# Kernel optimization log

Measured on AMD Instinct MI355X. Metric: run time of the kernel, lower is better.

The kernel has to match this reference:

```python
import jax, jax.numpy as jnp
import numpy as np

NEG_SLOPE = 0.2


def setup_inputs() -> dict:
    key = jax.random.key(0)
    kx, ka, kW, kav = jax.random.split(key, 4)
    B, V, H, D = 8, 2048, 256, 128
    x = jax.random.normal(kx, (B, V, H), dtype=jnp.float32)
    adjacency_matrix = jax.random.randint(ka, (V, V), 0, 2, dtype=jnp.int32)
    W = jax.random.normal(kW, (D, H), dtype=jnp.float32) * 0.05  # Linear(H->D), weight [out,in]
    a = jax.random.normal(kav, (1, 2 * D), dtype=jnp.float32) * 0.05  # Linear(2D->1)
    return {"x": x, "adjacency_matrix": adjacency_matrix, "W": W, "a": a}


def reference(x, adjacency_matrix, W, a):
    B, V, H = x.shape
    D = W.shape[0]
    # p = W(x): [B,V,D]
    p = jnp.einsum('bvh,dh->bvd', x, W)
    # a(cat(p_i, p_j)) == a_left.p_i + a_right.p_j ; leaky_relu applied to the sum (same math,
    # avoids materializing the O(B*V^2*2D) repeat/concat tensor)
    a_left, a_right = a[0, :D], a[0, D:]
    e_i = p @ a_left    # [B,V]
    e_j = p @ a_right   # [B,V]
    scores = jax.nn.leaky_relu(e_i[:, :, None] + e_j[:, None, :], negative_slope=NEG_SLOPE)  # [B,V,V]
    weights = jax.nn.softmax(scores, axis=-1)
    adj = adjacency_matrix.astype(weights.dtype)[None]  # [1,V,V]
    weights_masked = weights * adj
    # renormalize masked weights to the (unmasked) row mass
    weights_masked = weights_masked * (
        jnp.sum(weights, axis=-1, keepdims=True) / jnp.sum(weights_masked, axis=-1, keepdims=True)
    )
    # weighted sum over neighbors j: sum_j w[b,i,j] * p[b,j,:]
    attentioned = jnp.einsum('bij,bjd->bid', weights_masked, p)
    return jax.nn.relu(attentioned)
```

## Files before the change

### kernel.cpp

```cpp
#include <hip/hip_runtime.h>
#include <hip/hip_bf16.h>

#define BATCH 8
#define V 2048
#define H 256
#define D 128

typedef __attribute__((ext_vector_type(8))) _Float16 f16x8;
typedef __attribute__((ext_vector_type(4))) float f32x4;
typedef unsigned int uint32;

static __device__ __forceinline__ uint32 pk2(float lo, float hi) {
  __fp16 __attribute__((ext_vector_type(2))) h = __builtin_amdgcn_cvt_pkrtz(lo, hi);
  uint32 u;
  __builtin_memcpy(&u, &h, 4);
  return u;
}

__global__ __launch_bounds__(256) void k_pack(const int* __restrict__ adj,
                                              const float* __restrict__ W,
                                              const float* __restrict__ a,
                                              unsigned int* __restrict__ pkT,
                                              float* __restrict__ vL,
                                              float* __restrict__ vR) {
  const int blk = blockIdx.x;
  if (blk < V) {
    const int w = threadIdx.x >> 6, lane = threadIdx.x & 63;
    const int* row = adj + (size_t)blk * V;
#pragma unroll
    for (int it = 0; it < 8; ++it) {
      const int j = it * 256 + w * 64 + lane;
      unsigned long long m = __ballot(row[j] != 0);
      if (lane < 2) {
        const int jw = it * 8 + w * 2 + lane;
        pkT[(size_t)jw * V + blk] = (unsigned int)(m >> (lane * 32));
      }
    }
  } else {
    const int h = threadIdx.x;
    float sL = 0.f, sR = 0.f;
    for (int d = 0; d < D; ++d) {
      const float wv = W[(size_t)d * H + h];
      sL += wv * a[d];
      sR += wv * a[D + d];
    }
    vL[h] = sL;
    vR[h] = sR;
  }
}

#define DOT4(s, xv, vv) \
  s += (xv).x * (vv).x + (xv).y * (vv).y + (xv).z * (vv).z + (xv).w * (vv).w;

__global__ __launch_bounds__(256, 2) void k_proj(const float* __restrict__ x,
                                                 const float* __restrict__ W,
                                                 const float* __restrict__ vL,
                                                 const float* __restrict__ vR,
                                                 _Float16* __restrict__ pTf,
                                                 float* __restrict__ ei,
                                                 _Float16* __restrict__ Fh,
                                                 _Float16* __restrict__ Ph) {
  __shared__ _Float16 st[128][52];
  const int t = threadIdx.x, lane = t & 63, wave = t >> 6;
  const int b = blockIdx.x >> 6;
  const int j0 = (blockIdx.x & 63) * 32;
  const int kq = lane >> 4, l15 = lane & 15;

  const float* wrow0 = W + (size_t)(wave * 32 + l15) * H + kq * 8;
  const float* wrow1 = wrow0 + 16 * H;
  const float* xrow0 = x + ((size_t)(b * V + j0 + l15)) * H + kq * 8;
  const float* xrow1 = xrow0 + 16 * H;
  const float* vLp = vL + kq * 8;
  const float* vRp = vR + kq * 8;

  f32x4 acc[2][2];
#pragma unroll
  for (int i_ = 0; i_ < 2; ++i_)
#pragma unroll
    for (int j_ = 0; j_ < 2; ++j_) acc[i_][j_] = (f32x4){0.f, 0.f, 0.f, 0.f};
  float eL0 = 0.f, eL1 = 0.f, eR0 = 0.f, eR1 = 0.f;

  typedef union { uint32 u[4]; f16x8 v; } AFu_;
#pragma unroll
  for (int ks = 0; ks < 8; ++ks) {
    const int ho = ks * 32;
    const float4 w0a = *(const float4*)(wrow0 + ho), w0b = *(const float4*)(wrow0 + ho + 4);
    const float4 w1a = *(const float4*)(wrow1 + ho), w1b = *(const float4*)(wrow1 + ho + 4);
    const float4 x0a = *(const float4*)(xrow0 + ho), x0b = *(const float4*)(xrow0 + ho + 4);
    const float4 x1a = *(const float4*)(xrow1 + ho), x1b = *(const float4*)(xrow1 + ho + 4);
    AFu_ aw0, aw1, bx0, bx1;
    aw0.u[0] = pk2(w0a.x, w0a.y); aw0.u[1] = pk2(w0a.z, w0a.w);
    aw0.u[2] = pk2(w0b.x, w0b.y); aw0.u[3] = pk2(w0b.z, w0b.w);
    aw1.u[0] = pk2(w1a.x, w1a.y); aw1.u[1] = pk2(w1a.z, w1a.w);
    aw1.u[2] = pk2(w1b.x, w1b.y); aw1.u[3] = pk2(w1b.z, w1b.w);
    bx0.u[0] = pk2(x0a.x, x0a.y); bx0.u[1] = pk2(x0a.z, x0a.w);
    bx0.u[2] = pk2(x0b.x, x0b.y); bx0.u[3] = pk2(x0b.z, x0b.w);
    bx1.u[0] = pk2(x1a.x, x1a.y); bx1.u[1] = pk2(x1a.z, x1a.w);
    bx1.u[2] = pk2(x1b.x, x1b.y); bx1.u[3] = pk2(x1b.z, x1b.w);
    acc[0][0] = __builtin_amdgcn_mfma_f32_16x16x32_f16(aw0.v, bx0.v, acc[0][0], 0, 0, 0);
    acc[0][1] = __builtin_amdgcn_mfma_f32_16x16x32_f16(aw0.v, bx1.v, acc[0][1], 0, 0, 0);
    acc[1][0] = __builtin_amdgcn_mfma_f32_16x16x32_f16(aw1.v, bx0.v, acc[1][0], 0, 0, 0);
    acc[1][1] = __builtin_amdgcn_mfma_f32_16x16x32_f16(aw1.v, bx1.v, acc[1][1], 0, 0, 0);
    if (wave == 0) {
      const float4 vla = *(const float4*)(vLp + ho), vlb = *(const float4*)(vLp + ho + 4);
      const float4 vra = *(const float4*)(vRp + ho), vrb = *(const float4*)(vRp + ho + 4);
      DOT4(eL0, x0a, vla) DOT4(eL0, x0b, vlb)
      DOT4(eL1, x1a, vla) DOT4(eL1, x1b, vlb)
      DOT4(eR0, x0a, vra) DOT4(eR0, x0b, vrb)
      DOT4(eR1, x1a, vra) DOT4(eR1, x1b, vrb)
    }
  }

  if (wave == 0) {
    eL0 += __shfl_xor(eL0, 16, 64); eL0 += __shfl_xor(eL0, 32, 64);
    eL1 += __shfl_xor(eL1, 16, 64); eL1 += __shfl_xor(eL1, 32, 64);
    eR0 += __shfl_xor(eR0, 16, 64); eR0 += __shfl_xor(eR0, 32, 64);
    eR1 += __shfl_xor(eR1, 16, 64); eR1 += __shfl_xor(eR1, 32, 64);
    if (lane < 16) {
      const size_t r0 = (size_t)b * V + j0 + lane;
      ei[r0] = eL0;
      Fh[r0] = (_Float16)__expf(eR0);
      Ph[r0] = (_Float16)__expf(0.2f * eR0);
      const size_t r1 = r0 + 16;
      ei[r1] = eL1;
      Fh[r1] = (_Float16)__expf(eR1);
      Ph[r1] = (_Float16)__expf(0.2f * eR1);
    }
  }

#pragma unroll
  for (int t_ = 0; t_ < 2; ++t_)
#pragma unroll
    for (int jt = 0; jt < 2; ++jt)
#pragma unroll
      for (int r = 0; r < 4; ++r)
        st[(wave * 2 + t_) * 16 + kq * 4 + r][jt * 16 + l15] = (_Float16)acc[t_][jt][r];
  __syncthreads();

  const int c = (blockIdx.x & 63) >> 1;
  const int ks = blockIdx.x & 1;
  const int g = t >> 6;
#pragma unroll
  for (int ff = 0; ff < 2; ++ff) {
    const int dt = ff * 4 + g;
    const int dR = dt * 16 + l15;
    const int jc = kq * 8;
    union { unsigned long long ll[2]; f16x8 v; } vv_;
    vv_.ll[0] = *(const unsigned long long*)&st[dR][jc];
    vv_.ll[1] = *(const unsigned long long*)&st[dR][jc + 4];
    *(f16x8*)((char*)pTf +
              (((((size_t)b * 32 + c) * 8 + dt) * 2 + ks) * 64 + lane) * 16) = vv_.v;
  }
}


typedef union { uint4 v; uint32 u[4]; } U4;
typedef union { uint32 u[4]; f16x8 v; } AFu;
struct PFS {
  U4 FH0, FH1, PH0, PH1;
  uint32 w[2][2];
  AFu AF[2][2];
};

#define PKMUL(d, a, b) asm("v_pk_mul_f16 %0, %1, %2" : "=v"(d) : "v"(a), "v"(b));
#define PKMAX(d, a, b) asm("v_pk_max_f16 %0, %1, %2" : "=v"(d) : "v"(a), "v"(b));

#define WGEN(S)                                                        \
  _Pragma("unroll") for (int ig_ = 0; ig_ < 2; ++ig_) {                \
    const uint32 E2_ = Ei2g[ig_], EP2_ = Eip2g[ig_];                   \
    _Pragma("unroll") for (int ks_ = 0; ks_ < 2; ++ks_) {              \
      U4 M_;                                                           \
      M_.v = lut[((S).w[ig_][ks_] >> kq8) & 0xFF];                     \
      const U4& FH_ = ks_ ? (S).FH1 : (S).FH0;                         \
      const U4& PH_ = ks_ ? (S).PH1 : (S).PH0;                         \
      _Pragma("unroll") for (int p_ = 0; p_ < 4; ++p_) {               \
        uint32 t0_, t1_;                                               \
        PKMUL(t0_, E2_, FH_.u[p_])                                     \
        PKMUL(t1_, EP2_, PH_.u[p_])                                    \
        PKMAX(t0_, t0_, t1_)                                           \
        (S).AF[ig_][ks_].u[p_] = t0_ & M_.u[p_];                       \
      }                                                                \
    }                                                                  \
  }

#define PFETCH(S, C)                                       \
  {                                                        \
    const char* f_ = fbase + (C) * 128 + kq16;             \
    const char* p_ = pbase + (C) * 128 + kq16;             \
    (S).FH0.v = *(const uint4*)(f_);                       \
    (S).FH1.v = *(const uint4*)(f_ + 64);                  \
    (S).PH0.v = *(const uint4*)(p_);                       \
    (S).PH1.v = *(const uint4*)(p_ + 64);                  \
    (S).w[0][0] = adjpT[(size_t)((C) * 2) * V + iR0];      \
    (S).w[0][1] = adjpT[(size_t)((C) * 2 + 1) * V + iR0];  \
    (S).w[1][0] = adjpT[(size_t)((C) * 2) * V + iR1];      \
    (S).w[1][1] = adjpT[(size_t)((C) * 2 + 1) * V + iR1];  \
  }

#define LOADB(BR, C)                                      \
  {                                                       \
    const char* g_ = gbase + (size_t)(C) * 16384;         \
    _Pragma("unroll") for (int q_ = 0; q_ < 4; ++q_)      \
      BR[q_] = *(const f16x8*)(g_ + q_ * 1024);           \
  }

#define DOMFMA(S, BX)                                                          \
  _Pragma("unroll") for (int ig_ = 0; ig_ < 2; ++ig_)                          \
    _Pragma("unroll") for (int nt_ = 0; nt_ < 2; ++nt_)                        \
      _Pragma("unroll") for (int ks_ = 0; ks_ < 2; ++ks_)                      \
        acc[ig_][nt_][ks_] = __builtin_amdgcn_mfma_f32_16x16x32_f16(           \
            (S).AF[ig_][ks_].v, BX[nt_ * 2 + ks_], acc[ig_][nt_][ks_], 0, 0, 0); \
  _Pragma("unroll") for (int ig_ = 0; ig_ < 2; ++ig_)                          \
    _Pragma("unroll") for (int ks_ = 0; ks_ < 2; ++ks_)                        \
      accS[ig_][ks_] = __builtin_amdgcn_mfma_f32_16x16x32_f16(                 \
          (S).AF[ig_][ks_].v, onesv, accS[ig_][ks_], 0, 0, 0);

#define BODYF(C, SX, BX, SY)   \
  {                            \
    DOMFMA(SX, BX)             \
    WGEN(SY)                   \
    LOADB(BX, (C) + 2)         \
    PFETCH(SX, (C) + 2)        \
  }

__global__ __launch_bounds__(256, 2) void k_attn(
    const _Float16* __restrict__ pTf,
    const float* __restrict__ ei,
    const _Float16* __restrict__ Fht,
    const _Float16* __restrict__ Pht,
    const unsigned int* __restrict__ adjpT,
    float* __restrict__ out) {
  __shared__ uint4 lut[256];
  {
    const int tb = threadIdx.x;
    const uint32 m0 = ((tb & 1) ? 0xFFFFu : 0u) | ((tb & 2) ? 0xFFFF0000u : 0u);
    const uint32 m1 = ((tb & 4) ? 0xFFFFu : 0u) | ((tb & 8) ? 0xFFFF0000u : 0u);
    const uint32 m2 = ((tb & 16) ? 0xFFFFu : 0u) | ((tb & 32) ? 0xFFFF0000u : 0u);
    const uint32 m3 = ((tb & 64) ? 0xFFFFu : 0u) | ((tb & 128) ? 0xFFFF0000u : 0u);
    lut[tb] = make_uint4(m0, m1, m2, m3);
  }
  __syncthreads();

  const int t = threadIdx.x, lane = t & 63, wave = t >> 6;
  const int ih = wave >> 1;
  const int dq = wave & 1;
  const int pay = (blockIdx.x & 7) * 64 + (blockIdx.x >> 3);
  const int bdh = pay >> 4;
  const int itl = pay & 15;
  const int b = bdh >> 2, dh = (bdh >> 1) & 1;
  const int it = ((bdh & 1) << 4) | itl;
  const int i0b = it * 64;
  const int kq = lane >> 4;
  const int kq8 = kq * 8;
  const int kq16 = kq * 16;
  const int l15 = lane & 15;
  const int ibase = i0b + ih * 32;
  const int iR0 = ibase + l15;
  const int iR1 = iR0 + 16;

  const float eiv0 = ei[(size_t)b * V + iR0];
  const float eiv1 = ei[(size_t)b * V + iR1];
  uint32 Ei2g[2], Eip2g[2];
  {
    const float e0 = __expf(eiv0), e1 = __expf(eiv1);
    const float p0 = __expf(0.2f * eiv0), p1 = __expf(0.2f * eiv1);
    Ei2g[0] = pk2(e0, e0); Ei2g[1] = pk2(e1, e1);
    Eip2g[0] = pk2(p0, p0); Eip2g[1] = pk2(p1, p1);
  }
  const char* fbase = (const char*)(Fht + (size_t)b * V);
  const char* pbase = (const char*)(Pht + (size_t)b * V);
  const size_t fb0 = ((size_t)b * 32) * 16384 + (size_t)dh * 8192;
  const char* gbase = (const char*)pTf + fb0 + dq * 4096 + lane * 16;

  union { uint32 u[4]; f16x8 v; } ones_;
  ones_.u[0] = ones_.u[1] = ones_.u[2] = ones_.u[3] = 0x3C003C00u;
  const f16x8 onesv = ones_.v;

  f32x4 acc[2][2][2];
#pragma unroll
  for (int a_ = 0; a_ < 2; ++a_)
#pragma unroll
    for (int b_ = 0; b_ < 2; ++b_)
#pragma unroll
      for (int c_ = 0; c_ < 2; ++c_) acc[a_][b_][c_] = (f32x4){0.f, 0.f, 0.f, 0.f};
  f32x4 accS[2][2];
#pragma unroll
  for (int a_ = 0; a_ < 2; ++a_)
#pragma unroll
    for (int c_ = 0; c_ < 2; ++c_) accS[a_][c_] = (f32x4){0.f, 0.f, 0.f, 0.f};

  f16x8 bA[4], bB[4];
  PFS sA, sB;

  LOADB(bA, 0)
  LOADB(bB, 1)
  PFETCH(sA, 0)
  PFETCH(sB, 1)
  WGEN(sA)

  for (int c2 = 0; c2 < 15; ++c2) {
    const int c = c2 * 2;
    BODYF(c, sA, bA, sB)
    BODYF(c + 1, sB, bB, sA)
  }
  {
    DOMFMA(sA, bA)
    WGEN(sB)
  }
  { DOMFMA(sB, bB) }

  float* ob = out + ((size_t)b * V + ibase) * D + dh * 64 + dq * 32 + l15;
#pragma unroll
  for (int ig = 0; ig < 2; ++ig) {
#pragma unroll
    for (int r = 0; r < 4; ++r) {
      const float inv_ = 1.0f / (accS[ig][0][r] + accS[ig][1][r]);
#pragma unroll
      for (int nt = 0; nt < 2; ++nt) {
        const float v = (acc[ig][nt][0][r] + acc[ig][nt][1][r]) * inv_;
        ob[(size_t)(ig * 16 + kq * 4 + r) * D + nt * 16] = fmaxf(v, 0.f);
      }
    }
  }
}

extern "C" void kernel_launch(void* const* d_in, const int* in_sizes, int n_in,
                              void* d_out, int out_size, void* d_ws, size_t ws_size,
                              hipStream_t stream) {
  const float* x = (const float*)d_in[0];
  const int* adj = (const int*)d_in[1];
  const float* W = (const float*)d_in[2];
  const float* a = (const float*)d_in[3];
  float* out = (float*)d_out;

  char* ws = (char*)d_ws;
  _Float16* pTf = (_Float16*)ws;
  float* ei = (float*)(ws + (4u << 20));
  _Float16* Fh = (_Float16*)(ws + (4u << 20) + 65536);
  _Float16* Ph = (_Float16*)(ws + (4u << 20) + 98304);
  unsigned int* adjpT = (unsigned int*)(ws + (4u << 20) + 131072);
  float* vL = (float*)(ws + (4u << 20) + 131072 + 524288);
  float* vR = (float*)(ws + (4u << 20) + 131072 + 524288 + 1024);

  k_pack<<<dim3(V + 1), dim3(256), 0, stream>>>(adj, W, a, adjpT, vL, vR);
  k_proj<<<dim3(BATCH * (V / 32)), dim3(256), 0, stream>>>(x, W, vL, vR, pTf, ei, Fh, Ph);
  k_attn<<<dim3(BATCH * 2 * (V / 64)), dim3(256), 0, stream>>>(pTf, ei, Fh, Ph, adjpT, out);
}
```

Before: 54.69 us.

## Stage x in swizzled LDS, pre-convert W to fp16, shrink attention tiles

k_pack gains an extra block that converts W to fp16 once, so k_proj loads fp16 W fragments and no longer converts W per block. k_proj loads x coalesced into an XOR-swizzled LDS tile, computing the e_i/e_j dot products with full-wave reductions during staging. k_attn now gives each wave its own 16-column slice of a 32-row tile, with twice as many blocks, and computes the weight fragments just before use instead of software-pipelining them. Occupancy is raised to 4 blocks per CU, which trades recomputing the masked-weight fragments in every wave for lower register pressure and more parallelism.

```diff
diff --git a/kernel.cpp b/kernel.cpp
--- a/kernel.cpp
+++ b/kernel.cpp
@@ -22,7 +22,8 @@
                                               const float* __restrict__ a,
                                               unsigned int* __restrict__ pkT,
                                               float* __restrict__ vL,
-                                              float* __restrict__ vR) {
+                                              float* __restrict__ vR,
+                                              _Float16* __restrict__ Wh) {
   const int blk = blockIdx.x;
   if (blk < V) {
     const int w = threadIdx.x >> 6, lane = threadIdx.x & 63;
@@ -36,7 +37,7 @@
         pkT[(size_t)jw * V + blk] = (unsigned int)(m >> (lane * 32));
       }
     }
-  } else {
+  } else if (blk == V) {
     const int h = threadIdx.x;
     float sL = 0.f, sR = 0.f;
     for (int d = 0; d < D; ++d) {
@@ -46,86 +47,80 @@
     }
     vL[h] = sL;
     vR[h] = sR;
-  }
-}
-
-#define DOT4(s, xv, vv) \
-  s += (xv).x * (vv).x + (xv).y * (vv).y + (xv).z * (vv).z + (xv).w * (vv).w;
+  } else {
+    const int t = threadIdx.x;
+    for (int i = 0; i < D; ++i)
+      Wh[(size_t)i * H + t] = (_Float16)W[(size_t)i * H + t];
+  }
+}
 
 __global__ __launch_bounds__(256, 2) void k_proj(const float* __restrict__ x,
-                                                 const float* __restrict__ W,
+                                                 const _Float16* __restrict__ Wh,
                                                  const float* __restrict__ vL,
                                                  const float* __restrict__ vR,
                                                  _Float16* __restrict__ pTf,
                                                  float* __restrict__ ei,
                                                  _Float16* __restrict__ Fh,
                                                  _Float16* __restrict__ Ph) {
+  __shared__ char xls[32 * 512];
   __shared__ _Float16 st[128][52];
   const int t = threadIdx.x, lane = t & 63, wave = t >> 6;
   const int b = blockIdx.x >> 6;
-  const int j0 = (blockIdx.x & 63) * 32;
+  const int jt0 = blockIdx.x & 63;
+  const int j0 = jt0 * 32;
   const int kq = lane >> 4, l15 = lane & 15;
 
-  const float* wrow0 = W + (size_t)(wave * 32 + l15) * H + kq * 8;
-  const float* wrow1 = wrow0 + 16 * H;
-  const float* xrow0 = x + ((size_t)(b * V + j0 + l15)) * H + kq * 8;
-  const float* xrow1 = xrow0 + 16 * H;
-  const float* vLp = vL + kq * 8;
-  const float* vRp = vR + kq * 8;
+  {
+    const float4 vl4 = *(const float4*)(vL + lane * 4);
+    const float4 vr4 = *(const float4*)(vR + lane * 4);
+#pragma unroll
+    for (int rr = 0; rr < 8; ++rr) {
+      const int row = wave * 8 + rr;
+      const float4 xv = *(const float4*)(x + ((size_t)(b * V + j0 + row)) * H + lane * 4);
+      uint32 u0 = pk2(xv.x, xv.y), u1 = pk2(xv.z, xv.w);
+      const int off = row * 512 + ((lane * 8) ^ ((row & 7) << 4));
+      *(uint32*)(xls + off) = u0;
+      *(uint32*)(xls + off + 4) = u1;
+      float eL = xv.x * vl4.x + xv.y * vl4.y + xv.z * vl4.z + xv.w * vl4.w;
+      float eR = xv.x * vr4.x + xv.y * vr4.y + xv.z * vr4.z + xv.w * vr4.w;
+#pragma unroll
+      for (int off_ = 1; off_ < 64; off_ <<= 1) {
+        eL += __shfl_xor(eL, off_, 64);
+        eR += __shfl_xor(eR, off_, 64);
+      }
+      if (lane == 0) {
+        const size_t r_ = (size_t)b * V + j0 + row;
+        ei[r_] = eL;
+        Fh[r_] = (_Float16)__expf(eR);
+        Ph[r_] = (_Float16)__expf(0.2f * eR);
+      }
+    }
+  }
+  __syncthreads();
 
   f32x4 acc[2][2];
 #pragma unroll
   for (int i_ = 0; i_ < 2; ++i_)
 #pragma unroll
     for (int j_ = 0; j_ < 2; ++j_) acc[i_][j_] = (f32x4){0.f, 0.f, 0.f, 0.f};
-  float eL0 = 0.f, eL1 = 0.f, eR0 = 0.f, eR1 = 0.f;
-
-  typedef union { uint32 u[4]; f16x8 v; } AFu_;
+
+  const char* wbase = (const char*)Wh + ((size_t)(wave * 32 + l15) * H + kq * 8) * 2;
 #pragma unroll
   for (int ks = 0; ks < 8; ++ks) {
-    const int ho = ks * 32;
-    const float4 w0a = *(const float4*)(wrow0 + ho), w0b = *(const float4*)(wrow0 + ho + 4);
-    const float4 w1a = *(const float4*)(wrow1 + ho), w1b = *(const float4*)(wrow1 + ho + 4);
-    const float4 x0a = *(const float4*)(xrow0 + ho), x0b = *(const float4*)(xrow0 + ho + 4);
-    const float4 x1a = *(const float4*)(xrow1 + ho), x1b = *(const float4*)(xrow1 + ho + 4);
-    AFu_ aw0, aw1, bx0, bx1;
-    aw0.u[0] = pk2(w0a.x, w0a.y); aw0.u[1] = pk2(w0a.z, w0a.w);
-    aw0.u[2] = pk2(w0b.x, w0b.y); aw0.u[3] = pk2(w0b.z, w0b.w);
-    aw1.u[0] = pk2(w1a.x, w1a.y); aw1.u[1] = pk2(w1a.z, w1a.w);
-    aw1.u[2] = pk2(w1b.x, w1b.y); aw1.u[3] = pk2(w1b.z, w1b.w);
-    bx0.u[0] = pk2(x0a.x, x0a.y); bx0.u[1] = pk2(x0a.z, x0a.w);
-    bx0.u[2] = pk2(x0b.x, x0b.y); bx0.u[3] = pk2(x0b.z, x0b.w);
-    bx1.u[0] = pk2(x1a.x, x1a.y); bx1.u[1] = pk2(x1a.z, x1a.w);
-    bx1.u[2] = pk2(x1b.x, x1b.y); bx1.u[3] = pk2(x1b.z, x1b.w);
-    acc[0][0] = __builtin_amdgcn_mfma_f32_16x16x32_f16(aw0.v, bx0.v, acc[0][0], 0, 0, 0);
-    acc[0][1] = __builtin_amdgcn_mfma_f32_16x16x32_f16(aw0.v, bx1.v, acc[0][1], 0, 0, 0);
-    acc[1][0] = __builtin_amdgcn_mfma_f32_16x16x32_f16(aw1.v, bx0.v, acc[1][0], 0, 0, 0);
-    acc[1][1] = __builtin_amdgcn_mfma_f32_16x16x32_f16(aw1.v, bx1.v, acc[1][1], 0, 0, 0);
-    if (wave == 0) {
-      const float4 vla = *(const float4*)(vLp + ho), vlb = *(const float4*)(vLp + ho + 4);
-      const float4 vra = *(const float4*)(vRp + ho), vrb = *(const float4*)(vRp + ho + 4);
-      DOT4(eL0, x0a, vla) DOT4(eL0, x0b, vlb)
-      DOT4(eL1, x1a, vla) DOT4(eL1, x1b, vlb)
-      DOT4(eR0, x0a, vra) DOT4(eR0, x0b, vrb)
-      DOT4(eR1, x1a, vra) DOT4(eR1, x1b, vrb)
-    }
-  }
-
-  if (wave == 0) {
-    eL0 += __shfl_xor(eL0, 16, 64); eL0 += __shfl_xor(eL0, 32, 64);
-    eL1 += __shfl_xor(eL1, 16, 64); eL1 += __shfl_xor(eL1, 32, 64);
-    eR0 += __shfl_xor(eR0, 16, 64); eR0 += __shfl_xor(eR0, 32, 64);
-    eR1 += __shfl_xor(eR1, 16, 64); eR1 += __shfl_xor(eR1, 32, 64);
-    if (lane < 16) {
-      const size_t r0 = (size_t)b * V + j0 + lane;
-      ei[r0] = eL0;
-      Fh[r0] = (_Float16)__expf(eR0);
-      Ph[r0] = (_Float16)__expf(0.2f * eR0);
-      const size_t r1 = r0 + 16;
-      ei[r1] = eL1;
-      Fh[r1] = (_Float16)__expf(eR1);
-      Ph[r1] = (_Float16)__expf(0.2f * eR1);
-    }
+    f16x8 aw[2], bx[2];
+#pragma unroll
+    for (int t_ = 0; t_ < 2; ++t_)
+      aw[t_] = *(const f16x8*)(wbase + (t_ * 16 * H + ks * 32) * 2);
+#pragma unroll
+    for (int jt = 0; jt < 2; ++jt) {
+      const int row = jt * 16 + l15;
+      bx[jt] = *(const f16x8*)(xls + row * 512 + ((ks * 64 + kq * 16) ^ ((l15 & 7) << 4)));
+    }
+#pragma unroll
+    for (int t_ = 0; t_ < 2; ++t_)
+#pragma unroll
+      for (int jt = 0; jt < 2; ++jt)
+        acc[t_][jt] = __builtin_amdgcn_mfma_f32_16x16x32_f16(aw[t_], bx[jt], acc[t_][jt], 0, 0, 0);
   }
 
 #pragma unroll
@@ -137,8 +132,8 @@
         st[(wave * 2 + t_) * 16 + kq * 4 + r][jt * 16 + l15] = (_Float16)acc[t_][jt][r];
   __syncthreads();
 
-  const int c = (blockIdx.x & 63) >> 1;
-  const int ks = blockIdx.x & 1;
+  const int c = jt0 >> 1;
+  const int ksh = jt0 & 1;
   const int g = t >> 6;
 #pragma unroll
   for (int ff = 0; ff < 2; ++ff) {
@@ -149,28 +144,26 @@
     vv_.ll[0] = *(const unsigned long long*)&st[dR][jc];
     vv_.ll[1] = *(const unsigned long long*)&st[dR][jc + 4];
     *(f16x8*)((char*)pTf +
-              (((((size_t)b * 32 + c) * 8 + dt) * 2 + ks) * 64 + lane) * 16) = vv_.v;
-  }
-}
-
+              (((((size_t)b * 32 + c) * 8 + dt) * 2 + ksh) * 64 + lane) * 16) = vv_.v;
+  }
+}
 
 typedef union { uint4 v; uint32 u[4]; } U4;
 typedef union { uint32 u[4]; f16x8 v; } AFu;
 struct PFS {
   U4 FH0, FH1, PH0, PH1;
   uint32 w[2][2];
-  AFu AF[2][2];
 };
 
 #define PKMUL(d, a, b) asm("v_pk_mul_f16 %0, %1, %2" : "=v"(d) : "v"(a), "v"(b));
 #define PKMAX(d, a, b) asm("v_pk_max_f16 %0, %1, %2" : "=v"(d) : "v"(a), "v"(b));
 
-#define WGEN(S)                                                        \
+#define WGENX(S, AF_)                                                  \
   _Pragma("unroll") for (int ig_ = 0; ig_ < 2; ++ig_) {                \
     const uint32 E2_ = Ei2g[ig_], EP2_ = Eip2g[ig_];                   \
     _Pragma("unroll") for (int ks_ = 0; ks_ < 2; ++ks_) {              \
       U4 M_;                                                           \
-      M_.v = lut[((S).w[ig_][ks_] >> kq8) & 0xFF];                     \
+      M_.v = lut[(((S).w[ig_][ks_]) >> kq8) & 0xFF];                   \
       const U4& FH_ = ks_ ? (S).FH1 : (S).FH0;                         \
       const U4& PH_ = ks_ ? (S).PH1 : (S).PH0;                         \
       _Pragma("unroll") for (int p_ = 0; p_ < 4; ++p_) {               \
@@ -178,52 +171,58 @@
         PKMUL(t0_, E2_, FH_.u[p_])                                     \
         PKMUL(t1_, EP2_, PH_.u[p_])                                    \
         PKMAX(t0_, t0_, t1_)                                           \
-        (S).AF[ig_][ks_].u[p_] = t0_ & M_.u[p_];                       \
+        AF_[ig_][ks_].u[p_] = t0_ & M_.u[p_];                          \
       }                                                                \
     }                                                                  \
   }
 
-#define PFETCH(S, C)                                       \
-  {                                                        \
-    const char* f_ = fbase + (C) * 128 + kq16;             \
-    const char* p_ = pbase + (C) * 128 + kq16;             \
-    (S).FH0.v = *(const uint4*)(f_);                       \
-    (S).FH1.v = *(const uint4*)(f_ + 64);                  \
-    (S).PH0.v = *(const uint4*)(p_);                       \
-    (S).PH1.v = *(const uint4*)(p_ + 64);                  \
-    (S).w[0][0] = adjpT[(size_t)((C) * 2) * V + iR0];      \
-    (S).w[0][1] = adjpT[(size_t)((C) * 2 + 1) * V + iR0];  \
-    (S).w[1][0] = adjpT[(size_t)((C) * 2) * V + iR1];      \
-    (S).w[1][1] = adjpT[(size_t)((C) * 2 + 1) * V + iR1];  \
-  }
-
-#define LOADB(BR, C)                                      \
-  {                                                       \
-    const char* g_ = gbase + (size_t)(C) * 16384;         \
-    _Pragma("unroll") for (int q_ = 0; q_ < 4; ++q_)      \
-      BR[q_] = *(const f16x8*)(g_ + q_ * 1024);           \
-  }
-
-#define DOMFMA(S, BX)                                                          \
+#define PFETCH(S, C)                                           \
+  {                                                            \
+    const char* f_ = fbase + (C) * 128 + kq16;                 \
+    const char* p_ = pbase + (C) * 128 + kq16;                 \
+    (S).FH0.v = *(const uint4*)(f_);                           \
+    (S).FH1.v = *(const uint4*)(f_ + 64);                      \
+    (S).PH0.v = *(const uint4*)(p_);                           \
+    (S).PH1.v = *(const uint4*)(p_ + 64);                      \
+    (S).w[0][0] = adjpT[(size_t)((C) * 2) * V + iR0];          \
+    (S).w[0][1] = adjpT[(size_t)((C) * 2 + 1) * V + iR0];      \
+    (S).w[1][0] = adjpT[(size_t)((C) * 2) * V + iR1];          \
+    (S).w[1][1] = adjpT[(size_t)((C) * 2 + 1) * V + iR1];      \
+  }
+
+#define LOADB(BR, C)                                  \
+  {                                                   \
+    const char* g_ = gbase + (size_t)(C) * 16384;     \
+    BR[0] = *(const f16x8*)(g_);                      \
+    BR[1] = *(const f16x8*)(g_ + 1024);               \
+  }
+
+#define DOMFMA(AF_, BX)                                                        \
   _Pragma("unroll") for (int ig_ = 0; ig_ < 2; ++ig_)                          \
-    _Pragma("unroll") for (int nt_ = 0; nt_ < 2; ++nt_)                        \
-      _Pragma("unroll") for (int ks_ = 0; ks_ < 2; ++ks_)                      \
-        acc[ig_][nt_][ks_] = __builtin_amdgcn_mfma_f32_16x16x32_f16(           \
-            (S).AF[ig_][ks_].v, BX[nt_ * 2 + ks_], acc[ig_][nt_][ks_], 0, 0, 0); \
-  _Pragma("unroll") for (int ig_ = 0; ig_ < 2; ++ig_)                          \
-    _Pragma("unroll") for (int ks_ = 0; ks_ < 2; ++ks_)                        \
+    _Pragma("unroll") for (int ks_ = 0; ks_ < 2; ++ks_) {                      \
+      acc[ig_][ks_] = __builtin_amdgcn_mfma_f32_16x16x32_f16(                  \
+          AF_[ig_][ks_].v, BX[ks_], acc[ig_][ks_], 0, 0, 0);                   \
       accS[ig_][ks_] = __builtin_amdgcn_mfma_f32_16x16x32_f16(                 \
-          (S).AF[ig_][ks_].v, onesv, accS[ig_][ks_], 0, 0, 0);
-
-#define BODYF(C, SX, BX, SY)   \
-  {                            \
-    DOMFMA(SX, BX)             \
-    WGEN(SY)                   \
-    LOADB(BX, (C) + 2)         \
-    PFETCH(SX, (C) + 2)        \
-  }
-
-__global__ __launch_bounds__(256, 2) void k_attn(
+          AF_[ig_][ks_].v, onesv, accS[ig_][ks_], 0, 0, 0);                    \
+    }
+
+#define BODYF(C, S, BX)       \
+  {                           \
+    AFu af_[2][2];            \
+    WGENX(S, af_)             \
+    DOMFMA(af_, BX)           \
+    LOADB(BX, (C) + 2)        \
+    PFETCH(S, (C) + 2)        \
+  }
+
+#define BODYT(S, BX)          \
+  {                           \
+    AFu af_[2][2];            \
+    WGENX(S, af_)             \
+    DOMFMA(af_, BX)           \
+  }
+
+__global__ __launch_bounds__(256, 4) void k_attn(
     const _Float16* __restrict__ pTf,
     const float* __restrict__ ei,
     const _Float16* __restrict__ Fht,
@@ -241,21 +240,18 @@
   }
   __syncthreads();
 
-  const int t = threadIdx.x, lane = t & 63, wave = t >> 6;
-  const int ih = wave >> 1;
-  const int dq = wave & 1;
-  const int pay = (blockIdx.x & 7) * 64 + (blockIdx.x >> 3);
-  const int bdh = pay >> 4;
-  const int itl = pay & 15;
-  const int b = bdh >> 2, dh = (bdh >> 1) & 1;
-  const int it = ((bdh & 1) << 4) | itl;
-  const int i0b = it * 64;
+  const int t = threadIdx.x, lane = t & 63;
+  const int dq = t >> 6;
+  const int pay = (blockIdx.x & 7) * 128 + (blockIdx.x >> 3);
+  const int b = pay >> 7;
+  const int dh = (pay >> 6) & 1;
+  const int it = pay & 63;
+  const int i0 = it * 32;
   const int kq = lane >> 4;
   const int kq8 = kq * 8;
   const int kq16 = kq * 16;
   const int l15 = lane & 15;
-  const int ibase = i0b + ih * 32;
-  const int iR0 = ibase + l15;
+  const int iR0 = i0 + l15;
   const int iR1 = iR0 + 16;
 
   const float eiv0 = ei[(size_t)b * V + iR0];
@@ -269,57 +265,47 @@
   }
   const char* fbase = (const char*)(Fht + (size_t)b * V);
   const char* pbase = (const char*)(Pht + (size_t)b * V);
-  const size_t fb0 = ((size_t)b * 32) * 16384 + (size_t)dh * 8192;
-  const char* gbase = (const char*)pTf + fb0 + dq * 4096 + lane * 16;
+  const char* gbase = (const char*)pTf + ((size_t)b * 32) * 16384 +
+                      (size_t)(dh * 4 + dq) * 2048 + lane * 16;
 
   union { uint32 u[4]; f16x8 v; } ones_;
   ones_.u[0] = ones_.u[1] = ones_.u[2] = ones_.u[3] = 0x3C003C00u;
   const f16x8 onesv = ones_.v;
 
-  f32x4 acc[2][2][2];
+  f32x4 acc[2][2];
+  f32x4 accS[2][2];
 #pragma unroll
   for (int a_ = 0; a_ < 2; ++a_)
 #pragma unroll
-    for (int b_ = 0; b_ < 2; ++b_)
-#pragma unroll
-      for (int c_ = 0; c_ < 2; ++c_) acc[a_][b_][c_] = (f32x4){0.f, 0.f, 0.f, 0.f};
-  f32x4 accS[2][2];
-#pragma unroll
-  for (int a_ = 0; a_ < 2; ++a_)
-#pragma unroll
-    for (int c_ = 0; c_ < 2; ++c_) accS[a_][c_] = (f32x4){0.f, 0.f, 0.f, 0.f};
-
-  f16x8 bA[4], bB[4];
+    for (int c_ = 0; c_ < 2; ++c_) {
+      acc[a_][c_] = (f32x4){0.f, 0.f, 0.f, 0.f};
+      accS[a_][c_] = (f32x4){0.f, 0.f, 0.f, 0.f};
+    }
+
+  f16x8 bA[2], bB[2];
   PFS sA, sB;
 
   LOADB(bA, 0)
   LOADB(bB, 1)
   PFETCH(sA, 0)
   PFETCH(sB, 1)
-  WGEN(sA)
 
   for (int c2 = 0; c2 < 15; ++c2) {
     const int c = c2 * 2;
-    BODYF(c, sA, bA, sB)
-    BODYF(c + 1, sB, bB, sA)
-  }
-  {
-    DOMFMA(sA, bA)
-    WGEN(sB)
-  }
-  { DOMFMA(sB, bB) }
-
-  float* ob = out + ((size_t)b * V + ibase) * D + dh * 64 + dq * 32 + l15;
+    BODYF(c, sA, bA)
+    BODYF(c + 1, sB, bB)
+  }
+  BODYT(sA, bA)
+  BODYT(sB, bB)
+
+  float* ob = out + ((size_t)b * V + i0) * D + dh * 64 + dq * 16 + l15;
 #pragma unroll
   for (int ig = 0; ig < 2; ++ig) {
 #pragma unroll
     for (int r = 0; r < 4; ++r) {
       const float inv_ = 1.0f / (accS[ig][0][r] + accS[ig][1][r]);
-#pragma unroll
-      for (int nt = 0; nt < 2; ++nt) {
-        const float v = (acc[ig][nt][0][r] + acc[ig][nt][1][r]) * inv_;
-        ob[(size_t)(ig * 16 + kq * 4 + r) * D + nt * 16] = fmaxf(v, 0.f);
-      }
+      const float v = (acc[ig][0][r] + acc[ig][1][r]) * inv_;
+      ob[(size_t)(ig * 16 + kq * 4 + r) * D] = fmaxf(v, 0.f);
     }
   }
 }
@@ -339,10 +325,11 @@
   _Float16* Fh = (_Float16*)(ws + (4u << 20) + 65536);
   _Float16* Ph = (_Float16*)(ws + (4u << 20) + 98304);
   unsigned int* adjpT = (unsigned int*)(ws + (4u << 20) + 131072);
-  float* vL = (float*)(ws + (4u << 20) + 131072 + 524288);
-  float* vR = (float*)(ws + (4u << 20) + 131072 + 524288 + 1024);
-
-  k_pack<<<dim3(V + 1), dim3(256), 0, stream>>>(adj, W, a, adjpT, vL, vR);
-  k_proj<<<dim3(BATCH * (V / 32)), dim3(256), 0, stream>>>(x, W, vL, vR, pTf, ei, Fh, Ph);
-  k_attn<<<dim3(BATCH * 2 * (V / 64)), dim3(256), 0, stream>>>(pTf, ei, Fh, Ph, adjpT, out);
-}
+  float* vL = (float*)(ws + (4u << 20) + 655360);
+  float* vR = (float*)(ws + (4u << 20) + 656384);
+  _Float16* Wh = (_Float16*)(ws + (4u << 20) + 657408);
+
+  k_pack<<<dim3(V + 2), dim3(256), 0, stream>>>(adj, W, a, adjpT, vL, vR, Wh);
+  k_proj<<<dim3(BATCH * (V / 32)), dim3(256), 0, stream>>>(x, Wh, vL, vR, pTf, ei, Fh, Ph);
+  k_attn<<<dim3(BATCH * 2 * (V / 32)), dim3(256), 0, stream>>>(pTf, ei, Fh, Ph, adjpT, out);
+}
```

Result: slower. 68.65 us (+25.5%).

## Stage x tile in LDS, pre-convert W to fp16, replace mask LUT with bit math

Applied to the files above, without the earlier changes.

k_pack gains an extra block that converts W to fp16 once, so k_proj reads half-width weights. k_proj now loads each x row once with coalesced float4 loads, packs it to fp16 into a swizzled LDS tile, and computes the e_i/e_j dot products from that single load with a full-wave shuffle reduction. This removes the four-wave redundant global reads of x and the per-iteration fp32 to fp16 conversion. In k_attn, the shared-memory LUT for adjacency masks is replaced by bit shifts that build 0 or 2.0 in fp16 and a packed multiply, with the exp factors halved to compensate. That drops the LUT setup, its sync and the LDS lookups, at the cost of extra ALU ops per element.

```diff
diff --git a/kernel.cpp b/kernel.cpp
--- a/kernel.cpp
+++ b/kernel.cpp
@@ -22,7 +22,8 @@
                                               const float* __restrict__ a,
                                               unsigned int* __restrict__ pkT,
                                               float* __restrict__ vL,
-                                              float* __restrict__ vR) {
+                                              float* __restrict__ vR,
+                                              _Float16* __restrict__ Wh) {
   const int blk = blockIdx.x;
   if (blk < V) {
     const int w = threadIdx.x >> 6, lane = threadIdx.x & 63;
@@ -36,7 +37,7 @@
         pkT[(size_t)jw * V + blk] = (unsigned int)(m >> (lane * 32));
       }
     }
-  } else {
+  } else if (blk == V) {
     const int h = threadIdx.x;
     float sL = 0.f, sR = 0.f;
     for (int d = 0; d < D; ++d) {
@@ -46,86 +47,80 @@
     }
     vL[h] = sL;
     vR[h] = sR;
-  }
-}
-
-#define DOT4(s, xv, vv) \
-  s += (xv).x * (vv).x + (xv).y * (vv).y + (xv).z * (vv).z + (xv).w * (vv).w;
+  } else {
+    const int t = threadIdx.x;
+    for (int i = 0; i < D; ++i)
+      Wh[(size_t)i * H + t] = (_Float16)W[(size_t)i * H + t];
+  }
+}
 
 __global__ __launch_bounds__(256, 2) void k_proj(const float* __restrict__ x,
-                                                 const float* __restrict__ W,
+                                                 const _Float16* __restrict__ Wh,
                                                  const float* __restrict__ vL,
                                                  const float* __restrict__ vR,
                                                  _Float16* __restrict__ pTf,
                                                  float* __restrict__ ei,
                                                  _Float16* __restrict__ Fh,
                                                  _Float16* __restrict__ Ph) {
+  __shared__ char xls[32 * 512];
   __shared__ _Float16 st[128][52];
   const int t = threadIdx.x, lane = t & 63, wave = t >> 6;
   const int b = blockIdx.x >> 6;
-  const int j0 = (blockIdx.x & 63) * 32;
+  const int jt0 = blockIdx.x & 63;
+  const int j0 = jt0 * 32;
   const int kq = lane >> 4, l15 = lane & 15;
 
-  const float* wrow0 = W + (size_t)(wave * 32 + l15) * H + kq * 8;
-  const float* wrow1 = wrow0 + 16 * H;
-  const float* xrow0 = x + ((size_t)(b * V + j0 + l15)) * H + kq * 8;
-  const float* xrow1 = xrow0 + 16 * H;
-  const float* vLp = vL + kq * 8;
-  const float* vRp = vR + kq * 8;
+  {
+    const float4 vl4 = *(const float4*)(vL + lane * 4);
+    const float4 vr4 = *(const float4*)(vR + lane * 4);
+#pragma unroll
+    for (int rr = 0; rr < 8; ++rr) {
+      const int row = wave * 8 + rr;
+      const float4 xv = *(const float4*)(x + ((size_t)(b * V + j0 + row)) * H + lane * 4);
+      uint32 u0 = pk2(xv.x, xv.y), u1 = pk2(xv.z, xv.w);
+      const int off = row * 512 + ((lane * 8) ^ ((row & 7) << 4));
+      *(uint32*)(xls + off) = u0;
+      *(uint32*)(xls + off + 4) = u1;
+      float eL = xv.x * vl4.x + xv.y * vl4.y + xv.z * vl4.z + xv.w * vl4.w;
+      float eR = xv.x * vr4.x + xv.y * vr4.y + xv.z * vr4.z + xv.w * vr4.w;
+#pragma unroll
+      for (int off_ = 1; off_ < 64; off_ <<= 1) {
+        eL += __shfl_xor(eL, off_, 64);
+        eR += __shfl_xor(eR, off_, 64);
+      }
+      if (lane == 0) {
+        const size_t r_ = (size_t)b * V + j0 + row;
+        ei[r_] = eL;
+        Fh[r_] = (_Float16)__expf(eR);
+        Ph[r_] = (_Float16)__expf(0.2f * eR);
+      }
+    }
+  }
+  __syncthreads();
 
   f32x4 acc[2][2];
 #pragma unroll
   for (int i_ = 0; i_ < 2; ++i_)
 #pragma unroll
     for (int j_ = 0; j_ < 2; ++j_) acc[i_][j_] = (f32x4){0.f, 0.f, 0.f, 0.f};
-  float eL0 = 0.f, eL1 = 0.f, eR0 = 0.f, eR1 = 0.f;
-
-  typedef union { uint32 u[4]; f16x8 v; } AFu_;
+
+  const char* wbase = (const char*)Wh + ((size_t)(wave * 32 + l15) * H + kq * 8) * 2;
 #pragma unroll
   for (int ks = 0; ks < 8; ++ks) {
-    const int ho = ks * 32;
-    const float4 w0a = *(const float4*)(wrow0 + ho), w0b = *(const float4*)(wrow0 + ho + 4);
-    const float4 w1a = *(const float4*)(wrow1 + ho), w1b = *(const float4*)(wrow1 + ho + 4);
-    const float4 x0a = *(const float4*)(xrow0 + ho), x0b = *(const float4*)(xrow0 + ho + 4);
-    const float4 x1a = *(const float4*)(xrow1 + ho), x1b = *(const float4*)(xrow1 + ho + 4);
-    AFu_ aw0, aw1, bx0, bx1;
-    aw0.u[0] = pk2(w0a.x, w0a.y); aw0.u[1] = pk2(w0a.z, w0a.w);
-    aw0.u[2] = pk2(w0b.x, w0b.y); aw0.u[3] = pk2(w0b.z, w0b.w);
-    aw1.u[0] = pk2(w1a.x, w1a.y); aw1.u[1] = pk2(w1a.z, w1a.w);
-    aw1.u[2] = pk2(w1b.x, w1b.y); aw1.u[3] = pk2(w1b.z, w1b.w);
-    bx0.u[0] = pk2(x0a.x, x0a.y); bx0.u[1] = pk2(x0a.z, x0a.w);
-    bx0.u[2] = pk2(x0b.x, x0b.y); bx0.u[3] = pk2(x0b.z, x0b.w);
-    bx1.u[0] = pk2(x1a.x, x1a.y); bx1.u[1] = pk2(x1a.z, x1a.w);
-    bx1.u[2] = pk2(x1b.x, x1b.y); bx1.u[3] = pk2(x1b.z, x1b.w);
-    acc[0][0] = __builtin_amdgcn_mfma_f32_16x16x32_f16(aw0.v, bx0.v, acc[0][0], 0, 0, 0);
-    acc[0][1] = __builtin_amdgcn_mfma_f32_16x16x32_f16(aw0.v, bx1.v, acc[0][1], 0, 0, 0);
-    acc[1][0] = __builtin_amdgcn_mfma_f32_16x16x32_f16(aw1.v, bx0.v, acc[1][0], 0, 0, 0);
-    acc[1][1] = __builtin_amdgcn_mfma_f32_16x16x32_f16(aw1.v, bx1.v, acc[1][1], 0, 0, 0);
-    if (wave == 0) {
-      const float4 vla = *(const float4*)(vLp + ho), vlb = *(const float4*)(vLp + ho + 4);
-      const float4 vra = *(const float4*)(vRp + ho), vrb = *(const float4*)(vRp + ho + 4);
-      DOT4(eL0, x0a, vla) DOT4(eL0, x0b, vlb)
-      DOT4(eL1, x1a, vla) DOT4(eL1, x1b, vlb)
-      DOT4(eR0, x0a, vra) DOT4(eR0, x0b, vrb)
-      DOT4(eR1, x1a, vra) DOT4(eR1, x1b, vrb)
-    }
-  }
-
-  if (wave == 0) {
-    eL0 += __shfl_xor(eL0, 16, 64); eL0 += __shfl_xor(eL0, 32, 64);
-    eL1 += __shfl_xor(eL1, 16, 64); eL1 += __shfl_xor(eL1, 32, 64);
-    eR0 += __shfl_xor(eR0, 16, 64); eR0 += __shfl_xor(eR0, 32, 64);
-    eR1 += __shfl_xor(eR1, 16, 64); eR1 += __shfl_xor(eR1, 32, 64);
-    if (lane < 16) {
-      const size_t r0 = (size_t)b * V + j0 + lane;
-      ei[r0] = eL0;
-      Fh[r0] = (_Float16)__expf(eR0);
-      Ph[r0] = (_Float16)__expf(0.2f * eR0);
-      const size_t r1 = r0 + 16;
-      ei[r1] = eL1;
-      Fh[r1] = (_Float16)__expf(eR1);
-      Ph[r1] = (_Float16)__expf(0.2f * eR1);
-    }
+    f16x8 aw[2], bx[2];
+#pragma unroll
+    for (int t_ = 0; t_ < 2; ++t_)
+      aw[t_] = *(const f16x8*)(wbase + (t_ * 16 * H + ks * 32) * 2);
+#pragma unroll
+    for (int jt = 0; jt < 2; ++jt) {
+      const int row = jt * 16 + l15;
+      bx[jt] = *(const f16x8*)(xls + row * 512 + ((ks * 64 + kq * 16) ^ ((l15 & 7) << 4)));
+    }
+#pragma unroll
+    for (int t_ = 0; t_ < 2; ++t_)
+#pragma unroll
+      for (int jt = 0; jt < 2; ++jt)
+        acc[t_][jt] = __builtin_amdgcn_mfma_f32_16x16x32_f16(aw[t_], bx[jt], acc[t_][jt], 0, 0, 0);
   }
 
 #pragma unroll
@@ -137,8 +132,8 @@
         st[(wave * 2 + t_) * 16 + kq * 4 + r][jt * 16 + l15] = (_Float16)acc[t_][jt][r];
   __syncthreads();
 
-  const int c = (blockIdx.x & 63) >> 1;
-  const int ks = blockIdx.x & 1;
+  const int c = jt0 >> 1;
+  const int ksh = jt0 & 1;
   const int g = t >> 6;
 #pragma unroll
   for (int ff = 0; ff < 2; ++ff) {
@@ -149,7 +144,7 @@
     vv_.ll[0] = *(const unsigned long long*)&st[dR][jc];
     vv_.ll[1] = *(const unsigned long long*)&st[dR][jc + 4];
     *(f16x8*)((char*)pTf +
-              (((((size_t)b * 32 + c) * 8 + dt) * 2 + ks) * 64 + lane) * 16) = vv_.v;
+              (((((size_t)b * 32 + c) * 8 + dt) * 2 + ksh) * 64 + lane) * 16) = vv_.v;
   }
 }
 
@@ -169,16 +164,15 @@
   _Pragma("unroll") for (int ig_ = 0; ig_ < 2; ++ig_) {                \
     const uint32 E2_ = Ei2g[ig_], EP2_ = Eip2g[ig_];                   \
     _Pragma("unroll") for (int ks_ = 0; ks_ < 2; ++ks_) {              \
-      U4 M_;                                                           \
-      M_.v = lut[((S).w[ig_][ks_] >> kq8) & 0xFF];                     \
-      const U4& FH_ = ks_ ? (S).FH1 : (S).FH0;                         \
-      const U4& PH_ = ks_ ? (S).PH1 : (S).PH0;                         \
+      const uint32 sh_ = (S).w[ig_][ks_] >> kq8;                       \
       _Pragma("unroll") for (int p_ = 0; p_ < 4; ++p_) {               \
         uint32 t0_, t1_;                                               \
-        PKMUL(t0_, E2_, FH_.u[p_])                                     \
-        PKMUL(t1_, EP2_, PH_.u[p_])                                    \
+        PKMUL(t0_, E2_, (ks_ ? (S).FH1 : (S).FH0).u[p_])               \
+        PKMUL(t1_, EP2_, (ks_ ? (S).PH1 : (S).PH0).u[p_])              \
         PKMAX(t0_, t0_, t1_)                                           \
-        (S).AF[ig_][ks_].u[p_] = t0_ & M_.u[p_];                       \
+        const uint32 m_ = ((sh_ << (14 - 2 * p_)) & 0x4000u) |         \
+                          ((sh_ << (29 - 2 * p_)) & 0x40000000u);      \
+        PKMUL((S).AF[ig_][ks_].u[p_], t0_, m_)                         \
       }                                                                \
     }                                                                  \
   }
@@ -230,17 +224,6 @@
     const _Float16* __restrict__ Pht,
     const unsigned int* __restrict__ adjpT,
     float* __restrict__ out) {
-  __shared__ uint4 lut[256];
-  {
-    const int tb = threadIdx.x;
-    const uint32 m0 = ((tb & 1) ? 0xFFFFu : 0u) | ((tb & 2) ? 0xFFFF0000u : 0u);
-    const uint32 m1 = ((tb & 4) ? 0xFFFFu : 0u) | ((tb & 8) ? 0xFFFF0000u : 0u);
-    const uint32 m2 = ((tb & 16) ? 0xFFFFu : 0u) | ((tb & 32) ? 0xFFFF0000u : 0u);
-    const uint32 m3 = ((tb & 64) ? 0xFFFFu : 0u) | ((tb & 128) ? 0xFFFF0000u : 0u);
-    lut[tb] = make_uint4(m0, m1, m2, m3);
-  }
-  __syncthreads();
-
   const int t = threadIdx.x, lane = t & 63, wave = t >> 6;
   const int ih = wave >> 1;
   const int dq = wave & 1;
@@ -262,8 +245,8 @@
   const float eiv1 = ei[(size_t)b * V + iR1];
   uint32 Ei2g[2], Eip2g[2];
   {
-    const float e0 = __expf(eiv0), e1 = __expf(eiv1);
-    const float p0 = __expf(0.2f * eiv0), p1 = __expf(0.2f * eiv1);
+    const float e0 = 0.5f * __expf(eiv0), e1 = 0.5f * __expf(eiv1);
+    const float p0 = 0.5f * __expf(0.2f * eiv0), p1 = 0.5f * __expf(0.2f * eiv1);
     Ei2g[0] = pk2(e0, e0); Ei2g[1] = pk2(e1, e1);
     Eip2g[0] = pk2(p0, p0); Eip2g[1] = pk2(p1, p1);
   }
@@ -339,10 +322,11 @@
   _Float16* Fh = (_Float16*)(ws + (4u << 20) + 65536);
   _Float16* Ph = (_Float16*)(ws + (4u << 20) + 98304);
   unsigned int* adjpT = (unsigned int*)(ws + (4u << 20) + 131072);
-  float* vL = (float*)(ws + (4u << 20) + 131072 + 524288);
-  float* vR = (float*)(ws + (4u << 20) + 131072 + 524288 + 1024);
-
-  k_pack<<<dim3(V + 1), dim3(256), 0, stream>>>(adj, W, a, adjpT, vL, vR);
-  k_proj<<<dim3(BATCH * (V / 32)), dim3(256), 0, stream>>>(x, W, vL, vR, pTf, ei, Fh, Ph);
+  float* vL = (float*)(ws + (4u << 20) + 655360);
+  float* vR = (float*)(ws + (4u << 20) + 656384);
+  _Float16* Wh = (_Float16*)(ws + (4u << 20) + 657408);
+
+  k_pack<<<dim3(V + 2), dim3(256), 0, stream>>>(adj, W, a, adjpT, vL, vR, Wh);
+  k_proj<<<dim3(BATCH * (V / 32)), dim3(256), 0, stream>>>(x, Wh, vL, vR, pTf, ei, Fh, Ph);
   k_attn<<<dim3(BATCH * 2 * (V / 64)), dim3(256), 0, stream>>>(pTf, ei, Fh, Ph, adjpT, out);
 }
```

Result: no change. 54.46 us (median of 2 runs) (-0.4%).
